# Kernel optimization log

Hardware: AMD Instinct MI355X
Metric: run time of the kernel (lower is better)

## Reference

```python
import jax, jax.numpy as jnp
import numpy as np

EMBED = 1024
HEADS = 16
HEAD_DIM = EMBED // HEADS
N, L, S = 16, 256, 2


def setup_inputs() -> dict:
    key = jax.random.key(0)
    ks = jax.random.split(key, 9)
    values = jax.random.normal(ks[0], (N, L, EMBED, S), dtype=jnp.float32)
    keys_ = jax.random.normal(ks[1], (N, L, EMBED, S), dtype=jnp.float32)
    query = jax.random.normal(ks[2], (N, L, EMBED, S), dtype=jnp.float32)
    mask = jax.random.randint(ks[3], (N, S, EMBED, L), 0, 2, dtype=jnp.int32)
    # nn.Linear weights: y = x @ W.T (+ b)
    sc = 1.0 / np.sqrt(HEAD_DIM)
    Wv = jax.random.uniform(ks[4], (HEAD_DIM, HEAD_DIM), jnp.float32, -sc, sc)
    Wk = jax.random.uniform(ks[5], (HEAD_DIM, HEAD_DIM), jnp.float32, -sc, sc)
    Wq = jax.random.uniform(ks[6], (HEAD_DIM, HEAD_DIM), jnp.float32, -sc, sc)
    so = 1.0 / np.sqrt(EMBED)
    Wo = jax.random.uniform(ks[7], (EMBED, EMBED), jnp.float32, -so, so)
    bo = jax.random.uniform(ks[8], (EMBED,), jnp.float32, -so, so)
    return {"values": values, "keys": keys_, "query": query, "mask": mask,
            "Wv": Wv, "Wk": Wk, "Wq": Wq, "Wo": Wo, "bo": bo}


def reference(values, keys, query, mask, Wv, Wk, Wq, Wo, bo):
    n, L, E, S = values.shape
    H, D = HEADS, HEAD_DIM
    # reshape exactly as torch (memory reinterpretation): (n, len, S, H, D)
    v = values.reshape(n, L, S, H, D)
    k = keys.reshape(n, L, S, H, D)
    q = query.reshape(n, L, S, H, D)
    # per-head linear projections (no bias): x @ W.T
    v = jnp.einsum('nlshd,ed->nlshe', v, Wv)
    k = jnp.einsum('nlshd,ed->nlshe', k, Wk)
    q = jnp.einsum('nlshd,ed->nlshe', q, Wq)
    energy = jnp.einsum('nqshd,nkshd->nhsqk', q, k)
    # mask: (n, S, E, L) -> take feature 0 -> (n, S, L) -> repeat heads -> (n, H, S, L)
    m = mask.reshape(n, S, E, L)[:, :, 0, :]              # (n, S, L)
    m = jnp.tile(m[..., None], (1, 1, 1, H))               # (n, S, L, H)
    m = m.reshape(n, H, S, L)                              # as torch reshape
    energy = jnp.where(m[..., None] == 0, jnp.float32(-1e20), energy)
    # NOTE: original softmaxes over dim=3 (query axis) — replicate faithfully
    att = jax.nn.softmax(energy / jnp.sqrt(jnp.float32(E)), axis=3)
    out = jnp.einsum('nhsql,nlshd->nqhds', att, v)         # (n, q, H, D, S)
    out = out.reshape(n, L, S, H * D)                      # torch-style reshape
    return jnp.einsum('nqse,fe->nqsf', out, Wo) + bo
```

## Files before the change

### kernel.cpp

```cpp
#include <hip/hip_runtime.h>


typedef __attribute__((ext_vector_type(8))) short bf16x8;
typedef __attribute__((ext_vector_type(4))) float f32x4;

__device__ inline ushort f2bf(float x) {
    uint u = __float_as_uint(x);
    u += 0x7FFFu + ((u >> 16) & 1u);
    return (ushort)(u >> 16);
}

__global__ __launch_bounds__(256) void k_wot(
    const float* __restrict__ Wo, ushort* __restrict__ Wb)
{
    const int f = blockIdx.x;
    const int e4 = threadIdx.x * 4;
    const int hr = e4 >> 7, sp = (e4 >> 6) & 1, d = e4 & 63;
    const float* wrow = Wo + (long)f * 1024 + hr * 128 + 2 * d + sp;
    ushort o[4] = {f2bf(wrow[0]), f2bf(wrow[2]), f2bf(wrow[4]), f2bf(wrow[6])};
    *(uint2*)(Wb + (long)f * 1024 + e4) = *(uint2*)o;
}

__global__ __launch_bounds__(512) void k_proj(
    const float* __restrict__ Av, const float* __restrict__ Ak,
    const float* __restrict__ Aq, const float* __restrict__ Wv,
    const float* __restrict__ Wk, const float* __restrict__ Wq,
    ushort* __restrict__ kB, ushort* __restrict__ qB,
    ushort* __restrict__ vB)
{
    __shared__ ushort Wsb[3][64][72];
    const int b = blockIdx.x;
    const int n = b >> 5, h = (b >> 1) & 15, s = b & 1;
    const float* Asrc[3] = {Av, Ak, Aq};
    const float* Wsrc[3] = {Wv, Wk, Wq};
    const int tid = threadIdx.x;
    const int wid = tid >> 6, lane = tid & 63;
    const int lr = lane & 15, lk = lane >> 4;

    const long abase = (long)n * 524288 + s * 1024 + h * 64;
    const long slice = ((long)((n * 16 + h) * 2 + s)) * 16384;
    ushort* Bdst[3] = {vB, kB, qB};

#pragma unroll
    for (int m = 0; m < 3; ++m)
#pragma unroll
        for (int w = 0; w < 2; ++w) {
            int idx = w * 512 + tid;
            int r = idx >> 4, c4 = (idx & 15) * 4;
            float4 v = *(const float4*)(Wsrc[m] + r * 64 + c4);
            ushort t4[4] = {f2bf(v.x), f2bf(v.y), f2bf(v.z), f2bf(v.w)};
            *(uint2*)&Wsb[m][r][c4] = *(uint2*)t4;
        }
    __syncthreads();

    const int l0 = wid * 32;
#pragma unroll 1
    for (int m = 0; m < 3; ++m) {
        const float* A = Asrc[m];
        ushort* B = Bdst[m];
#pragma unroll
        for (int lt = 0; lt < 2; ++lt) {
            const int lrow = l0 + lt * 16 + lr;
            const float* arow = A + abase + (long)lrow * 2048;
            bf16x8 bfrag[2];
#pragma unroll
            for (int ks = 0; ks < 2; ++ks) {
                float4 v0 = *(const float4*)(arow + ks * 32 + lk * 8);
                float4 v1 = *(const float4*)(arow + ks * 32 + lk * 8 + 4);
                ushort t8[8] = {f2bf(v0.x), f2bf(v0.y), f2bf(v0.z), f2bf(v0.w),
                                f2bf(v1.x), f2bf(v1.y), f2bf(v1.z), f2bf(v1.w)};
                bfrag[ks] = *(bf16x8*)t8;
            }
#pragma unroll
            for (int et = 0; et < 4; ++et) {
                f32x4 acc;
#pragma unroll
                for (int rg = 0; rg < 4; ++rg) acc[rg] = 0.f;
#pragma unroll
                for (int ks = 0; ks < 2; ++ks) {
                    bf16x8 wfrag = *(const bf16x8*)
                        &Wsb[m][et * 16 + lr][ks * 32 + lk * 8];
                    acc = __builtin_amdgcn_mfma_f32_16x16x32_bf16(
                        wfrag, bfrag[ks], acc, 0, 0, 0);
                }
                ushort t4[4] = {f2bf(acc[0]), f2bf(acc[1]),
                                f2bf(acc[2]), f2bf(acc[3])};
                *(uint2*)(B + slice + (long)lrow * 64 + et * 16 + lk * 4) =
                    *(uint2*)t4;
            }
        }
    }
}

__global__ __launch_bounds__(512) void k_attn(
    const ushort* __restrict__ kB, const ushort* __restrict__ qB,
    const ushort* __restrict__ vB, const int* __restrict__ mask,
    ushort* __restrict__ Xb)
{
    __shared__ ushort Ks[32][72];
    __shared__ ushort vsT[64][44];
    __shared__ ushort Es[128][44];
    __shared__ float Zl[256];
    __shared__ int mb16[16];
    const int nhs = blockIdx.x;
    const int n = nhs >> 5, h = (nhs >> 1) & 15, s = nhs & 1;
    const long slice = (long)nhs * 16384;
    const int tid = threadIdx.x;
    const int wid = tid >> 6, lane = tid & 63;
    const int lr = lane & 15, lk = lane >> 4;

    bf16x8 aq[2][2];
#pragma unroll
    for (int qt = 0; qt < 2; ++qt) {
        const int qb = wid * 32 + qt * 16;
        aq[qt][0] = *(const bf16x8*)(qB + slice + (qb + lr) * 64 + lk * 8);
        aq[qt][1] = *(const bf16x8*)(qB + slice + (qb + lr) * 64 + 32 + lk * 8);
    }
    const int mrow = n * 524288 + (h >> 3) * 262144 + (h & 7) * 32 + s * 16;
    if (tid < 16) mb16[tid] = mask[mrow + tid];
    if (tid < 256) Zl[tid] = 0.f;

    const float scale = 0.03125f;

#pragma unroll 1
    for (int sl = 0; sl < 8; ++sl) {
        __syncthreads();
        if (tid < 256) {
            int r = tid >> 3, c8 = (tid & 7) * 8;
            *(uint4*)&Ks[r][c8] =
                *(const uint4*)(kB + slice + (sl * 32 + r) * 64 + c8);
        }
        __syncthreads();

        float zlt[2] = {0.f, 0.f};
#pragma unroll
        for (int qt = 0; qt < 2; ++qt) {
            const int qb = wid * 32 + qt * 16;
            if (mb16[qb >> 4] == 0) continue;
#pragma unroll
            for (int lt = 0; lt < 2; ++lt) {
                f32x4 sacc;
#pragma unroll
                for (int rg = 0; rg < 4; ++rg) sacc[rg] = 0.f;
                bf16x8 b0 = *(const bf16x8*)&Ks[lt * 16 + lr][lk * 8];
                bf16x8 b1 = *(const bf16x8*)&Ks[lt * 16 + lr][32 + lk * 8];
                sacc = __builtin_amdgcn_mfma_f32_16x16x32_bf16(
                    aq[qt][0], b0, sacc, 0, 0, 0);
                sacc = __builtin_amdgcn_mfma_f32_16x16x32_bf16(
                    aq[qt][1], b1, sacc, 0, 0, 0);
#pragma unroll
                for (int rg = 0; rg < 4; ++rg)
                    zlt[lt] += __expf(sacc[rg] * scale);
            }
        }
#pragma unroll
        for (int lt = 0; lt < 2; ++lt) {
            float v = zlt[lt];
            v += __shfl_xor(v, 16);
            v += __shfl_xor(v, 32);
            if (lk == 0)
                atomicAdd(&Zl[sl * 32 + lt * 16 + lr], v);
        }
    }

    __syncthreads();
    if (tid < 256) {
        float z = Zl[tid];
        Zl[tid] = (z > 0.f) ? 1.0f / z : 1.0f / 256.0f;
    }

    f32x4 acc0[4], acc1[4];
#pragma unroll
    for (int dt = 0; dt < 4; ++dt)
#pragma unroll
        for (int rg = 0; rg < 4; ++rg) { acc0[dt][rg] = 0.f; acc1[dt][rg] = 0.f; }

#pragma unroll 1
    for (int sl = 0; sl < 8; ++sl) {
        __syncthreads();
        if (tid < 256) {
            int r = tid >> 3, c8 = (tid & 7) * 8;
            *(uint4*)&Ks[r][c8] =
                *(const uint4*)(kB + slice + (sl * 32 + r) * 64 + c8);
        } else {
            int t = tid - 256;
            int l = t >> 3, d8 = (t & 7) * 8;
            uint4 vv = *(const uint4*)(vB + slice + (sl * 32 + l) * 64 + d8);
            ushort t8[8];
            *(uint4*)t8 = vv;
#pragma unroll
            for (int u = 0; u < 8; ++u) vsT[d8 + u][l] = t8[u];
        }
        __syncthreads();

#pragma unroll
        for (int qt = 0; qt < 2; ++qt) {
            const int qb = wid * 32 + qt * 16;
            const bool live = (mb16[qb >> 4] != 0);
#pragma unroll
            for (int lt = 0; lt < 2; ++lt) {
                f32x4 sacc;
#pragma unroll
                for (int rg = 0; rg < 4; ++rg) sacc[rg] = 0.f;
                bf16x8 b0 = *(const bf16x8*)&Ks[lt * 16 + lr][lk * 8];
                bf16x8 b1 = *(const bf16x8*)&Ks[lt * 16 + lr][32 + lk * 8];
                sacc = __builtin_amdgcn_mfma_f32_16x16x32_bf16(
                    aq[qt][0], b0, sacc, 0, 0, 0);
                sacc = __builtin_amdgcn_mfma_f32_16x16x32_bf16(
                    aq[qt][1], b1, sacc, 0, 0, 0);
                const int l = lt * 16 + lr;
                const float iz = Zl[sl * 32 + l];
#pragma unroll
                for (int rg = 0; rg < 4; ++rg) {
                    float ev = live ? __expf(sacc[rg] * scale) * iz : 0.f;
                    Es[wid * 16 + lk * 4 + rg][l] = f2bf(ev);
                }
            }
            __builtin_amdgcn_s_waitcnt(0);
            bf16x8 aP = *(const bf16x8*)&Es[wid * 16 + lr][lk * 8];
            f32x4* accp = (qt == 0) ? acc0 : acc1;
#pragma unroll
            for (int dt = 0; dt < 4; ++dt) {
                bf16x8 bV = *(const bf16x8*)&vsT[dt * 16 + lr][lk * 8];
                accp[dt] = __builtin_amdgcn_mfma_f32_16x16x32_bf16(
                    aP, bV, accp[dt], 0, 0, 0);
            }
        }
    }

#pragma unroll
    for (int qt = 0; qt < 2; ++qt) {
        const f32x4* accp = (qt == 0) ? acc0 : acc1;
        const int qb = wid * 32 + qt * 16;
#pragma unroll
        for (int dt = 0; dt < 4; ++dt) {
#pragma unroll
            for (int rg = 0; rg < 4; ++rg) {
                const int q = qb + lk * 4 + rg;
                const int d = dt * 16 + lr;
                Xb[slice + (long)q * 64 + d] = f2bf(accp[dt][rg]);
            }
        }
    }
}

__global__ __launch_bounds__(512) void k_wo(
    const ushort* __restrict__ Xb, const ushort* __restrict__ Wb,
    const float* __restrict__ bo, float* __restrict__ out)
{
    __shared__ ushort Xs[128][72];
    __shared__ ushort Ws[128][72];
    const int b = blockIdx.x;
    const int by = b >> 3, bx = b & 7;
    const int r0 = by * 128, f0 = bx * 128;
    const int tid = threadIdx.x;
    const int wid = tid >> 6, lane = tid & 63;
    const int wr = wid >> 2, wc = wid & 3;
    const int lr = lane & 15, lk = lane >> 4;

    f32x4 acc[4][2];
#pragma unroll
    for (int rt = 0; rt < 4; ++rt)
#pragma unroll
        for (int ft = 0; ft < 2; ++ft)
#pragma unroll
            for (int rg = 0; rg < 4; ++rg) acc[rt][ft][rg] = 0.f;

    const int sr = tid >> 2, sc = (tid & 3) * 16;
    const int sR = r0 + sr;
    const int sn = sR >> 9, sq = (sR >> 1) & 255, ss2 = sR & 1;

#pragma unroll 1
    for (int eo = 0; eo < 1024; eo += 64) {
        const int hr = eo >> 7, sp = (eo >> 6) & 1;
        __syncthreads();
        {
            long xo = ((long)((sn * 16 + (ss2 * 8 + hr)) * 2 + sp)) * 16384 +
                      sq * 64 + sc;
            *(uint4*)&Xs[sr][sc] = *(const uint4*)(Xb + xo);
            *(uint4*)&Xs[sr][sc + 8] = *(const uint4*)(Xb + xo + 8);
            long wo = (long)(f0 + sr) * 1024 + eo + sc;
            *(uint4*)&Ws[sr][sc] = *(const uint4*)(Wb + wo);
            *(uint4*)&Ws[sr][sc + 8] = *(const uint4*)(Wb + wo + 8);
        }
        __syncthreads();

#pragma unroll
        for (int ks = 0; ks < 2; ++ks) {
            bf16x8 a[4], bb[2];
#pragma unroll
            for (int rt = 0; rt < 4; ++rt)
                a[rt] = *(const bf16x8*)
                    &Xs[wr * 64 + rt * 16 + lr][ks * 32 + lk * 8];
#pragma unroll
            for (int ft = 0; ft < 2; ++ft)
                bb[ft] = *(const bf16x8*)
                    &Ws[wc * 32 + ft * 16 + lr][ks * 32 + lk * 8];
#pragma unroll
            for (int rt = 0; rt < 4; ++rt)
#pragma unroll
                for (int ft = 0; ft < 2; ++ft)
                    acc[rt][ft] = __builtin_amdgcn_mfma_f32_16x16x32_bf16(
                        a[rt], bb[ft], acc[rt][ft], 0, 0, 0);
        }
    }

#pragma unroll
    for (int ft = 0; ft < 2; ++ft) {
        const int f = f0 + wc * 32 + ft * 16 + lr;
        const float bias = bo[f];
#pragma unroll
        for (int rt = 0; rt < 4; ++rt) {
#pragma unroll
            for (int rg = 0; rg < 4; ++rg) {
                const int r = r0 + wr * 64 + rt * 16 + lk * 4 + rg;
                out[(long)r * 1024 + f] = acc[rt][ft][rg] + bias;
            }
        }
    }
}

extern "C" void kernel_launch(void* const* d_in, const int* in_sizes, int n_in,
                              void* d_out, int out_size, void* d_ws,
                              size_t ws_size, hipStream_t stream)
{
    const float* vals = (const float*)d_in[0];
    const float* keys = (const float*)d_in[1];
    const float* qrys = (const float*)d_in[2];
    const int*   mask = (const int*)d_in[3];
    const float* Wv   = (const float*)d_in[4];
    const float* Wk   = (const float*)d_in[5];
    const float* Wq   = (const float*)d_in[6];
    const float* Wo   = (const float*)d_in[7];
    const float* bo   = (const float*)d_in[8];
    float* ws  = (float*)d_ws;
    ushort* kB = (ushort*)(ws);
    ushort* qB = (ushort*)(ws + 4194304);
    ushort* vB = (ushort*)(ws + 8388608);
    ushort* Xb = (ushort*)(ws + 12582912);
    ushort* Wb = (ushort*)(ws + 16777216);
    float* out = (float*)d_out;

    k_wot <<<1024, 256, 0, stream>>>(Wo, Wb);
    k_proj<<< 512, 512, 0, stream>>>(vals, keys, qrys, Wv, Wk, Wq, kB, qB, vB);
    k_attn<<< 512, 512, 0, stream>>>(kB, qB, vB, mask, Xb);
    k_wo  <<< 512, 512, 0, stream>>>(Xb, Wb, bo, out);
}
```

Baseline: 97.45 us.

## Fuse Q/K/V projections into attention kernel, dropping intermediate bf16 buffers

Removes the separate projection kernel and instead projects Q once into shared memory and recomputes K (twice) and V tiles on the fly inside each attention slice loop from fp32 inputs. This eliminates the global round trip of projected K/Q/V bf16 tensors and one kernel launch. The cost is redundant K projection work and fp32 input reads of keys in both passes, plus a reorganized shared-memory union layout.

```diff
diff --git a/kernel.cpp b/kernel.cpp
--- a/kernel.cpp
+++ b/kernel.cpp
@@ -21,47 +21,102 @@
     *(uint2*)(Wb + (long)f * 1024 + e4) = *(uint2*)o;
 }
 
-__global__ __launch_bounds__(512) void k_proj(
+#define WKS 0
+#define WVS 4608
+#define MBO 9216
+#define UNI 9248
+
+__global__ __launch_bounds__(512) void k_attn(
     const float* __restrict__ Av, const float* __restrict__ Ak,
     const float* __restrict__ Aq, const float* __restrict__ Wv,
     const float* __restrict__ Wk, const float* __restrict__ Wq,
-    ushort* __restrict__ kB, ushort* __restrict__ qB,
-    ushort* __restrict__ vB)
+    const int* __restrict__ mask, ushort* __restrict__ Xb)
 {
-    __shared__ ushort Wsb[3][64][72];
-    const int b = blockIdx.x;
-    const int n = b >> 5, h = (b >> 1) & 15, s = b & 1;
-    const float* Asrc[3] = {Av, Ak, Aq};
-    const float* Wsrc[3] = {Wv, Wk, Wq};
+    __shared__ ushort smem[32288];
+    ushort* Qp  = smem + UNI;
+    ushort* Wqs = smem + UNI + 18432;
+    ushort* Ks  = smem + UNI;
+    ushort* vsT = smem + UNI + 2304;
+    ushort* Es  = smem + UNI + 5120;
+    float*  Zl  = (float*)&smem[UNI + 10752];
+    int*    mb16 = (int*)&smem[MBO];
+
+    const int nhs = blockIdx.x;
+    const int n = nhs >> 5, h = (nhs >> 1) & 15, s = nhs & 1;
+    const long abase = (long)n * 524288 + s * 1024 + h * 64;
+    const long slice = (long)nhs * 16384;
     const int tid = threadIdx.x;
     const int wid = tid >> 6, lane = tid & 63;
     const int lr = lane & 15, lk = lane >> 4;
 
-    const long abase = (long)n * 524288 + s * 1024 + h * 64;
-    const long slice = ((long)((n * 16 + h) * 2 + s)) * 16384;
-    ushort* Bdst[3] = {vB, kB, qB};
-
-#pragma unroll
-    for (int m = 0; m < 3; ++m)
-#pragma unroll
-        for (int w = 0; w < 2; ++w) {
-            int idx = w * 512 + tid;
-            int r = idx >> 4, c4 = (idx & 15) * 4;
-            float4 v = *(const float4*)(Wsrc[m] + r * 64 + c4);
-            ushort t4[4] = {f2bf(v.x), f2bf(v.y), f2bf(v.z), f2bf(v.w)};
-            *(uint2*)&Wsb[m][r][c4] = *(uint2*)t4;
-        }
+#pragma unroll
+    for (int w = 0; w < 2; ++w) {
+        int idx = w * 512 + tid;
+        int r = idx >> 4, c4 = (idx & 15) * 4;
+        float4 vk = *(const float4*)(Wk + r * 64 + c4);
+        float4 vv = *(const float4*)(Wv + r * 64 + c4);
+        float4 vq = *(const float4*)(Wq + r * 64 + c4);
+        ushort tk[4] = {f2bf(vk.x), f2bf(vk.y), f2bf(vk.z), f2bf(vk.w)};
+        ushort tv[4] = {f2bf(vv.x), f2bf(vv.y), f2bf(vv.z), f2bf(vv.w)};
+        ushort tq[4] = {f2bf(vq.x), f2bf(vq.y), f2bf(vq.z), f2bf(vq.w)};
+        *(uint2*)&smem[WKS + r * 72 + c4] = *(uint2*)tk;
+        *(uint2*)&smem[WVS + r * 72 + c4] = *(uint2*)tv;
+        *(uint2*)&Wqs[r * 72 + c4] = *(uint2*)tq;
+    }
+    const int mrow = n * 524288 + (h >> 3) * 262144 + (h & 7) * 32 + s * 16;
+    if (tid < 16) mb16[tid] = mask[mrow + tid];
     __syncthreads();
 
-    const int l0 = wid * 32;
+#pragma unroll
+    for (int qt = 0; qt < 2; ++qt) {
+        const int qrow = wid * 32 + qt * 16 + lr;
+        const float* arow = Aq + abase + (long)qrow * 2048;
+        bf16x8 bfrag[2];
+#pragma unroll
+        for (int ks = 0; ks < 2; ++ks) {
+            float4 v0 = *(const float4*)(arow + ks * 32 + lk * 8);
+            float4 v1 = *(const float4*)(arow + ks * 32 + lk * 8 + 4);
+            ushort t8[8] = {f2bf(v0.x), f2bf(v0.y), f2bf(v0.z), f2bf(v0.w),
+                            f2bf(v1.x), f2bf(v1.y), f2bf(v1.z), f2bf(v1.w)};
+            bfrag[ks] = *(bf16x8*)t8;
+        }
+#pragma unroll
+        for (int et = 0; et < 4; ++et) {
+            f32x4 acc;
+#pragma unroll
+            for (int rg = 0; rg < 4; ++rg) acc[rg] = 0.f;
+#pragma unroll
+            for (int ks = 0; ks < 2; ++ks) {
+                bf16x8 wf = *(const bf16x8*)
+                    &Wqs[(et * 16 + lr) * 72 + ks * 32 + lk * 8];
+                acc = __builtin_amdgcn_mfma_f32_16x16x32_bf16(
+                    wf, bfrag[ks], acc, 0, 0, 0);
+            }
+            ushort t4[4] = {f2bf(acc[0]), f2bf(acc[1]),
+                            f2bf(acc[2]), f2bf(acc[3])};
+            *(uint2*)&Qp[qrow * 72 + et * 16 + lk * 4] = *(uint2*)t4;
+        }
+    }
+    __builtin_amdgcn_s_waitcnt(0);
+    bf16x8 aq[2][2];
+#pragma unroll
+    for (int qt = 0; qt < 2; ++qt) {
+        const int qb = wid * 32 + qt * 16;
+        aq[qt][0] = *(const bf16x8*)&Qp[(qb + lr) * 72 + lk * 8];
+        aq[qt][1] = *(const bf16x8*)&Qp[(qb + lr) * 72 + 32 + lk * 8];
+    }
+    __syncthreads();
+    if (tid < 256) Zl[tid] = 0.f;
+
+    const float scale = 0.03125f;
+    const int plt = wid >> 2, pet = wid & 3;
+
 #pragma unroll 1
-    for (int m = 0; m < 3; ++m) {
-        const float* A = Asrc[m];
-        ushort* B = Bdst[m];
-#pragma unroll
-        for (int lt = 0; lt < 2; ++lt) {
-            const int lrow = l0 + lt * 16 + lr;
-            const float* arow = A + abase + (long)lrow * 2048;
+    for (int sl = 0; sl < 8; ++sl) {
+        __syncthreads();
+        {
+            const int lrow = sl * 32 + plt * 16 + lr;
+            const float* arow = Ak + abase + (long)lrow * 2048;
             bf16x8 bfrag[2];
 #pragma unroll
             for (int ks = 0; ks < 2; ++ks) {
@@ -71,64 +126,20 @@
                                 f2bf(v1.x), f2bf(v1.y), f2bf(v1.z), f2bf(v1.w)};
                 bfrag[ks] = *(bf16x8*)t8;
             }
-#pragma unroll
-            for (int et = 0; et < 4; ++et) {
-                f32x4 acc;
-#pragma unroll
-                for (int rg = 0; rg < 4; ++rg) acc[rg] = 0.f;
-#pragma unroll
-                for (int ks = 0; ks < 2; ++ks) {
-                    bf16x8 wfrag = *(const bf16x8*)
-                        &Wsb[m][et * 16 + lr][ks * 32 + lk * 8];
-                    acc = __builtin_amdgcn_mfma_f32_16x16x32_bf16(
-                        wfrag, bfrag[ks], acc, 0, 0, 0);
-                }
-                ushort t4[4] = {f2bf(acc[0]), f2bf(acc[1]),
-                                f2bf(acc[2]), f2bf(acc[3])};
-                *(uint2*)(B + slice + (long)lrow * 64 + et * 16 + lk * 4) =
-                    *(uint2*)t4;
-            }
-        }
-    }
-}
-
-__global__ __launch_bounds__(512) void k_attn(
-    const ushort* __restrict__ kB, const ushort* __restrict__ qB,
-    const ushort* __restrict__ vB, const int* __restrict__ mask,
-    ushort* __restrict__ Xb)
-{
-    __shared__ ushort Ks[32][72];
-    __shared__ ushort vsT[64][44];
-    __shared__ ushort Es[128][44];
-    __shared__ float Zl[256];
-    __shared__ int mb16[16];
-    const int nhs = blockIdx.x;
-    const int n = nhs >> 5, h = (nhs >> 1) & 15, s = nhs & 1;
-    const long slice = (long)nhs * 16384;
-    const int tid = threadIdx.x;
-    const int wid = tid >> 6, lane = tid & 63;
-    const int lr = lane & 15, lk = lane >> 4;
-
-    bf16x8 aq[2][2];
-#pragma unroll
-    for (int qt = 0; qt < 2; ++qt) {
-        const int qb = wid * 32 + qt * 16;
-        aq[qt][0] = *(const bf16x8*)(qB + slice + (qb + lr) * 64 + lk * 8);
-        aq[qt][1] = *(const bf16x8*)(qB + slice + (qb + lr) * 64 + 32 + lk * 8);
-    }
-    const int mrow = n * 524288 + (h >> 3) * 262144 + (h & 7) * 32 + s * 16;
-    if (tid < 16) mb16[tid] = mask[mrow + tid];
-    if (tid < 256) Zl[tid] = 0.f;
-
-    const float scale = 0.03125f;
-
-#pragma unroll 1
-    for (int sl = 0; sl < 8; ++sl) {
-        __syncthreads();
-        if (tid < 256) {
-            int r = tid >> 3, c8 = (tid & 7) * 8;
-            *(uint4*)&Ks[r][c8] =
-                *(const uint4*)(kB + slice + (sl * 32 + r) * 64 + c8);
+            f32x4 acc;
+#pragma unroll
+            for (int rg = 0; rg < 4; ++rg) acc[rg] = 0.f;
+#pragma unroll
+            for (int ks = 0; ks < 2; ++ks) {
+                bf16x8 wf = *(const bf16x8*)
+                    &smem[WKS + (pet * 16 + lr) * 72 + ks * 32 + lk * 8];
+                acc = __builtin_amdgcn_mfma_f32_16x16x32_bf16(
+                    wf, bfrag[ks], acc, 0, 0, 0);
+            }
+            ushort t4[4] = {f2bf(acc[0]), f2bf(acc[1]),
+                            f2bf(acc[2]), f2bf(acc[3])};
+            *(uint2*)&Ks[(plt * 16 + lr) * 72 + pet * 16 + lk * 4] =
+                *(uint2*)t4;
         }
         __syncthreads();
 
@@ -142,8 +153,10 @@
                 f32x4 sacc;
 #pragma unroll
                 for (int rg = 0; rg < 4; ++rg) sacc[rg] = 0.f;
-                bf16x8 b0 = *(const bf16x8*)&Ks[lt * 16 + lr][lk * 8];
-                bf16x8 b1 = *(const bf16x8*)&Ks[lt * 16 + lr][32 + lk * 8];
+                bf16x8 b0 = *(const bf16x8*)
+                    &Ks[(lt * 16 + lr) * 72 + lk * 8];
+                bf16x8 b1 = *(const bf16x8*)
+                    &Ks[(lt * 16 + lr) * 72 + 32 + lk * 8];
                 sacc = __builtin_amdgcn_mfma_f32_16x16x32_bf16(
                     aq[qt][0], b0, sacc, 0, 0, 0);
                 sacc = __builtin_amdgcn_mfma_f32_16x16x32_bf16(
@@ -178,18 +191,46 @@
 #pragma unroll 1
     for (int sl = 0; sl < 8; ++sl) {
         __syncthreads();
-        if (tid < 256) {
-            int r = tid >> 3, c8 = (tid & 7) * 8;
-            *(uint4*)&Ks[r][c8] =
-                *(const uint4*)(kB + slice + (sl * 32 + r) * 64 + c8);
-        } else {
-            int t = tid - 256;
-            int l = t >> 3, d8 = (t & 7) * 8;
-            uint4 vv = *(const uint4*)(vB + slice + (sl * 32 + l) * 64 + d8);
-            ushort t8[8];
-            *(uint4*)t8 = vv;
-#pragma unroll
-            for (int u = 0; u < 8; ++u) vsT[d8 + u][l] = t8[u];
+        {
+            const int lrow = sl * 32 + plt * 16 + lr;
+            const float* krow = Ak + abase + (long)lrow * 2048;
+            const float* vrow = Av + abase + (long)lrow * 2048;
+            bf16x8 kf[2], vf[2];
+#pragma unroll
+            for (int ks = 0; ks < 2; ++ks) {
+                float4 k0 = *(const float4*)(krow + ks * 32 + lk * 8);
+                float4 k1 = *(const float4*)(krow + ks * 32 + lk * 8 + 4);
+                float4 w0 = *(const float4*)(vrow + ks * 32 + lk * 8);
+                float4 w1 = *(const float4*)(vrow + ks * 32 + lk * 8 + 4);
+                ushort tk[8] = {f2bf(k0.x), f2bf(k0.y), f2bf(k0.z), f2bf(k0.w),
+                                f2bf(k1.x), f2bf(k1.y), f2bf(k1.z), f2bf(k1.w)};
+                ushort tv[8] = {f2bf(w0.x), f2bf(w0.y), f2bf(w0.z), f2bf(w0.w),
+                                f2bf(w1.x), f2bf(w1.y), f2bf(w1.z), f2bf(w1.w)};
+                kf[ks] = *(bf16x8*)tk;
+                vf[ks] = *(bf16x8*)tv;
+            }
+            f32x4 ka, va;
+#pragma unroll
+            for (int rg = 0; rg < 4; ++rg) { ka[rg] = 0.f; va[rg] = 0.f; }
+#pragma unroll
+            for (int ks = 0; ks < 2; ++ks) {
+                bf16x8 wfk = *(const bf16x8*)
+                    &smem[WKS + (pet * 16 + lr) * 72 + ks * 32 + lk * 8];
+                bf16x8 wfv = *(const bf16x8*)
+                    &smem[WVS + (pet * 16 + lr) * 72 + ks * 32 + lk * 8];
+                ka = __builtin_amdgcn_mfma_f32_16x16x32_bf16(
+                    wfk, kf[ks], ka, 0, 0, 0);
+                va = __builtin_amdgcn_mfma_f32_16x16x32_bf16(
+                    wfv, vf[ks], va, 0, 0, 0);
+            }
+            ushort t4[4] = {f2bf(ka[0]), f2bf(ka[1]),
+                            f2bf(ka[2]), f2bf(ka[3])};
+            *(uint2*)&Ks[(plt * 16 + lr) * 72 + pet * 16 + lk * 4] =
+                *(uint2*)t4;
+#pragma unroll
+            for (int rg = 0; rg < 4; ++rg)
+                vsT[(pet * 16 + lk * 4 + rg) * 44 + plt * 16 + lr] =
+                    f2bf(va[rg]);
         }
         __syncthreads();
 
@@ -202,8 +243,10 @@
                 f32x4 sacc;
 #pragma unroll
                 for (int rg = 0; rg < 4; ++rg) sacc[rg] = 0.f;
-                bf16x8 b0 = *(const bf16x8*)&Ks[lt * 16 + lr][lk * 8];
-                bf16x8 b1 = *(const bf16x8*)&Ks[lt * 16 + lr][32 + lk * 8];
+                bf16x8 b0 = *(const bf16x8*)
+                    &Ks[(lt * 16 + lr) * 72 + lk * 8];
+                bf16x8 b1 = *(const bf16x8*)
+                    &Ks[(lt * 16 + lr) * 72 + 32 + lk * 8];
                 sacc = __builtin_amdgcn_mfma_f32_16x16x32_bf16(
                     aq[qt][0], b0, sacc, 0, 0, 0);
                 sacc = __builtin_amdgcn_mfma_f32_16x16x32_bf16(
@@ -213,15 +256,16 @@
 #pragma unroll
                 for (int rg = 0; rg < 4; ++rg) {
                     float ev = live ? __expf(sacc[rg] * scale) * iz : 0.f;
-                    Es[wid * 16 + lk * 4 + rg][l] = f2bf(ev);
+                    Es[(wid * 16 + lk * 4 + rg) * 44 + l] = f2bf(ev);
                 }
             }
             __builtin_amdgcn_s_waitcnt(0);
-            bf16x8 aP = *(const bf16x8*)&Es[wid * 16 + lr][lk * 8];
+            bf16x8 aP = *(const bf16x8*)&Es[(wid * 16 + lr) * 44 + lk * 8];
             f32x4* accp = (qt == 0) ? acc0 : acc1;
 #pragma unroll
             for (int dt = 0; dt < 4; ++dt) {
-                bf16x8 bV = *(const bf16x8*)&vsT[dt * 16 + lr][lk * 8];
+                bf16x8 bV = *(const bf16x8*)
+                    &vsT[(dt * 16 + lr) * 44 + lk * 8];
                 accp[dt] = __builtin_amdgcn_mfma_f32_16x16x32_bf16(
                     aP, bV, accp[dt], 0, 0, 0);
             }
@@ -334,15 +378,11 @@
     const float* Wo   = (const float*)d_in[7];
     const float* bo   = (const float*)d_in[8];
     float* ws  = (float*)d_ws;
-    ushort* kB = (ushort*)(ws);
-    ushort* qB = (ushort*)(ws + 4194304);
-    ushort* vB = (ushort*)(ws + 8388608);
-    ushort* Xb = (ushort*)(ws + 12582912);
-    ushort* Wb = (ushort*)(ws + 16777216);
+    ushort* Xb = (ushort*)(ws);
+    ushort* Wb = (ushort*)(ws + 4194304);
     float* out = (float*)d_out;
 
     k_wot <<<1024, 256, 0, stream>>>(Wo, Wb);
-    k_proj<<< 512, 512, 0, stream>>>(vals, keys, qrys, Wv, Wk, Wq, kB, qB, vB);
-    k_attn<<< 512, 512, 0, stream>>>(kB, qB, vB, mask, Xb);
+    k_attn<<< 512, 512, 0, stream>>>(vals, keys, qrys, Wv, Wk, Wq, mask, Xb);
     k_wo  <<< 512, 512, 0, stream>>>(Xb, Wb, bo, out);
 }
```

Measured after the change: 120.8 us. 1.24x slower.

## Remap projection blocks to contiguous row chunks staged through shared memory

Applied to the files above, without the earlier changes.

The projection kernel now gives each block 16 consecutive L rows across all 16 heads for one (n, s), instead of one head over all 256 rows. Each input matrix chunk is loaded with fully coalesced float4 reads of contiguous 4 KB rows, converted to bf16 in shared memory, and then fed to the MFMAs. Previously each lane read strided 256-byte fragments. The cost is a larger LDS footprint and extra barriers per matrix.

```diff
diff --git a/kernel.cpp b/kernel.cpp
--- a/kernel.cpp
+++ b/kernel.cpp
@@ -28,18 +28,19 @@
     ushort* __restrict__ kB, ushort* __restrict__ qB,
     ushort* __restrict__ vB)
 {
+    __shared__ ushort As[16][1032];
     __shared__ ushort Wsb[3][64][72];
     const int b = blockIdx.x;
-    const int n = b >> 5, h = (b >> 1) & 15, s = b & 1;
+    const int n = b >> 5, s = (b >> 4) & 1, lc = b & 15;
+    const int l0 = lc * 16;
     const float* Asrc[3] = {Av, Ak, Aq};
     const float* Wsrc[3] = {Wv, Wk, Wq};
+    ushort* Bdst[3] = {vB, kB, qB};
     const int tid = threadIdx.x;
     const int wid = tid >> 6, lane = tid & 63;
     const int lr = lane & 15, lk = lane >> 4;
 
-    const long abase = (long)n * 524288 + s * 1024 + h * 64;
-    const long slice = ((long)((n * 16 + h) * 2 + s)) * 16384;
-    ushort* Bdst[3] = {vB, kB, qB};
+    const long rowbase = (long)n * 524288 + (long)l0 * 2048 + s * 1024;
 
 #pragma unroll
     for (int m = 0; m < 3; ++m)
@@ -51,26 +52,31 @@
             ushort t4[4] = {f2bf(v.x), f2bf(v.y), f2bf(v.z), f2bf(v.w)};
             *(uint2*)&Wsb[m][r][c4] = *(uint2*)t4;
         }
-    __syncthreads();
-
-    const int l0 = wid * 32;
+
 #pragma unroll 1
     for (int m = 0; m < 3; ++m) {
+        __syncthreads();
         const float* A = Asrc[m];
+#pragma unroll
+        for (int w = 0; w < 8; ++w) {
+            int idx = w * 512 + tid;
+            int r = idx >> 8, c4 = (idx & 255) * 4;
+            float4 v = *(const float4*)(A + rowbase + (long)r * 2048 + c4);
+            ushort t4[4] = {f2bf(v.x), f2bf(v.y), f2bf(v.z), f2bf(v.w)};
+            *(uint2*)&As[r][c4] = *(uint2*)t4;
+        }
+        __syncthreads();
+
         ushort* B = Bdst[m];
 #pragma unroll
-        for (int lt = 0; lt < 2; ++lt) {
-            const int lrow = l0 + lt * 16 + lr;
-            const float* arow = A + abase + (long)lrow * 2048;
+        for (int hh = 0; hh < 2; ++hh) {
+            const int h = wid * 2 + hh;
+            const long slice = ((long)((n * 16 + h) * 2 + s)) * 16384;
             bf16x8 bfrag[2];
 #pragma unroll
-            for (int ks = 0; ks < 2; ++ks) {
-                float4 v0 = *(const float4*)(arow + ks * 32 + lk * 8);
-                float4 v1 = *(const float4*)(arow + ks * 32 + lk * 8 + 4);
-                ushort t8[8] = {f2bf(v0.x), f2bf(v0.y), f2bf(v0.z), f2bf(v0.w),
-                                f2bf(v1.x), f2bf(v1.y), f2bf(v1.z), f2bf(v1.w)};
-                bfrag[ks] = *(bf16x8*)t8;
-            }
+            for (int ks = 0; ks < 2; ++ks)
+                bfrag[ks] = *(const bf16x8*)
+                    &As[lr][h * 64 + ks * 32 + lk * 8];
 #pragma unroll
             for (int et = 0; et < 4; ++et) {
                 f32x4 acc;
@@ -85,8 +91,8 @@
                 }
                 ushort t4[4] = {f2bf(acc[0]), f2bf(acc[1]),
                                 f2bf(acc[2]), f2bf(acc[3])};
-                *(uint2*)(B + slice + (long)lrow * 64 + et * 16 + lk * 4) =
-                    *(uint2*)t4;
+                *(uint2*)(B + slice + (long)(l0 + lr) * 64 +
+                          et * 16 + lk * 4) = *(uint2*)t4;
             }
         }
     }
```

Measured after the change: 101.3 us. +4.0%, slower.
